# Kernel tuning notes

Measured on AMD Instinct MI355X. Metric: run time of the kernel, lower is better.

Reference implementation:

```python
import math
import jax, jax.numpy as jnp
import numpy as np

B, S, D, H, L, V = 4, 1024, 1024, 16, 12, 32000
DH = D // H
MAX_LEN = 5000


def _layernorm(x, g, b, eps=1e-5):
    mu = jnp.mean(x, axis=-1, keepdims=True)
    var = jnp.mean(jnp.square(x - mu), axis=-1, keepdims=True)
    return (x - mu) * jax.lax.rsqrt(var + eps) * g + b


def _make_pe():
    pos = np.arange(MAX_LEN, dtype=np.float32)[:, None]
    div = np.exp(np.arange(0, D, 2, dtype=np.float32) * (-math.log(10000.0) / D))
    pe = np.zeros((MAX_LEN, D), dtype=np.float32)
    pe[:, 0::2] = np.sin(pos * div)
    pe[:, 1::2] = np.cos(pos * div)
    return jnp.asarray(pe[:, None, :])  # [max_len, 1, D] as in the torch buffer


def setup_inputs() -> dict:
    key = jax.random.key(0)
    ks = jax.random.split(key, 8)
    X = jax.random.randint(ks[0], (B, S), 0, V)
    emb = jax.random.normal(ks[1], (V, D), dtype=jnp.float32) * 0.02
    pe = _make_pe()
    ln1_g = jnp.ones((L, D), jnp.float32)
    ln1_b = jnp.zeros((L, D), jnp.float32)
    wa = jax.random.normal(ks[2], (L, D, 3 * D), dtype=jnp.float32) * 0.02
    ba = jnp.zeros((L, 3 * D), jnp.float32)
    wp = jax.random.normal(ks[3], (L, D, D), dtype=jnp.float32) * 0.02
    bp = jnp.zeros((L, D), jnp.float32)
    ln2_g = jnp.ones((L, D), jnp.float32)
    ln2_b = jnp.zeros((L, D), jnp.float32)
    wf = jax.random.normal(ks[4], (L, D, D), dtype=jnp.float32) * 0.02
    bf = jnp.zeros((L, D), jnp.float32)
    wout = jax.random.normal(ks[5], (V, D), dtype=jnp.float32) * 0.02
    return dict(X=X, emb=emb, pe=pe, ln1_g=ln1_g, ln1_b=ln1_b, wa=wa, ba=ba,
                wp=wp, bp=bp, ln2_g=ln2_g, ln2_b=ln2_b, wf=wf, bf=bf, wout=wout)


def _block(x, ln1g, ln1b, wa_i, ba_i, wp_i, bp_i, ln2g, ln2b, wf_i, bf_i):
    h = _layernorm(x, ln1g, ln1b)               # post-ln1 value is the residual base
    qkv = h @ wa_i + ba_i                        # [B,S,3D]
    q, k, v = jnp.split(qkv, 3, axis=-1)
    def heads(t):
        return t.reshape(B, S, H, DH).transpose(0, 2, 1, 3)  # [B,H,S,DH]
    q, k, v = heads(q), heads(k), heads(v)
    scores = jnp.einsum('bhqd,bhkd->bhqk', q, k)  # NOTE: no 1/sqrt(d) scaling (scale=False)
    probs = jax.nn.softmax(scores, axis=-1)
    o = jnp.einsum('bhqk,bhkd->bhqd', probs, v)
    o = o.transpose(0, 2, 1, 3).reshape(B, S, D)
    attn_out = o @ wp_i + bp_i
    x = h + attn_out
    x = x + _layernorm(x, ln2g, ln2b) @ wf_i + bf_i
    return x


def reference(X, emb, pe, ln1_g, ln1_b, wa, ba, wp, bp, ln2_g, ln2_b, wf, bf, wout):
    x = emb[X] * math.sqrt(D)           # [B,S,D]
    x = x + pe[:B]                       # faithful: pe indexed by batch dim, broadcast over seq
    for i in range(L):
        x = _block(x, ln1_g[i], ln1_b[i], wa[i], ba[i], wp[i], bp[i],
                   ln2_g[i], ln2_b[i], wf[i], bf[i])
    logits = jnp.einsum('bsd,vd->bsv', x, wout)  # Linear(d, vocab, bias=False)
    return logits
```

## Files before the change

### kernel.cpp

```cpp
#include <hip/hip_runtime.h>
#include <hip/hip_bf16.h>

typedef __attribute__((ext_vector_type(4))) float f32x4;
typedef __attribute__((ext_vector_type(8))) short s16x8;
typedef __attribute__((ext_vector_type(4))) short s16x4;

constexpr int Bc = 4, Sc = 1024, Dc = 1024, Hc = 16, DHc = 64, Lc = 12, Vc = 32000;
constexpr int Tc = Bc * Sc;
constexpr int D3c = 3 * Dc;

static __device__ __forceinline__ short f2bf(float f) {
  union { float f; unsigned u; } v; v.f = f;
  unsigned r = (v.u + 0x7FFFu + ((v.u >> 16) & 1u)) >> 16;
  return (short)r;
}

__launch_bounds__(256)
__global__ void k_embed(const int* __restrict__ X, const float* __restrict__ emb,
                        const float* __restrict__ pe, float* __restrict__ x) {
  int row = blockIdx.x;
  int b = row >> 10;
  int tok = X[row];
  int t = threadIdx.x;
  float4 e = ((const float4*)(emb + (size_t)tok * Dc))[t];
  float4 p = ((const float4*)(pe + (size_t)b * Dc))[t];
  float4 r;
  r.x = e.x * 32.0f + p.x;  r.y = e.y * 32.0f + p.y;
  r.z = e.z * 32.0f + p.z;  r.w = e.w * 32.0f + p.w;
  ((float4*)(x + (size_t)row * Dc))[t] = r;
}

template<bool WF32>
__launch_bounds__(256)
__global__ void k_ln(const float* __restrict__ x, const float* __restrict__ g,
                     const float* __restrict__ be, float* __restrict__ hf,
                     short* __restrict__ hb) {
  int row = blockIdx.x, t = threadIdx.x;
  float4 v = ((const float4*)(x + (size_t)row * Dc))[t];
  float s1 = v.x + v.y + v.z + v.w;
  float s2 = v.x * v.x + v.y * v.y + v.z * v.z + v.w * v.w;
#pragma unroll
  for (int off = 1; off < 64; off <<= 1) {
    s1 += __shfl_xor(s1, off);
    s2 += __shfl_xor(s2, off);
  }
  __shared__ float a1[4], a2[4];
  if ((t & 63) == 0) { a1[t >> 6] = s1; a2[t >> 6] = s2; }
  __syncthreads();
  s1 = a1[0] + a1[1] + a1[2] + a1[3];
  s2 = a2[0] + a2[1] + a2[2] + a2[3];
  float mu = s1 * (1.0f / Dc);
  float var = s2 * (1.0f / Dc) - mu * mu;
  float rs = rsqrtf(var + 1e-5f);
  float4 gg = ((const float4*)g)[t];
  float4 bb = ((const float4*)be)[t];
  float4 r;
  r.x = (v.x - mu) * rs * gg.x + bb.x;
  r.y = (v.y - mu) * rs * gg.y + bb.y;
  r.z = (v.z - mu) * rs * gg.z + bb.z;
  r.w = (v.w - mu) * rs * gg.w + bb.w;
  if (WF32) ((float4*)(hf + (size_t)row * Dc))[t] = r;
  s16x4 o; o[0] = f2bf(r.x); o[1] = f2bf(r.y); o[2] = f2bf(r.z); o[3] = f2bf(r.w);
  ((s16x4*)(hb + (size_t)row * Dc))[t] = o;
}

__launch_bounds__(256)
__global__ void k_transpose_bf(const float* __restrict__ in0, short* __restrict__ out0,
                               int R, int C) {
  const float* in = in0 + (size_t)blockIdx.z * R * C;
  short* out = out0 + (size_t)blockIdx.z * R * C;
  __shared__ float tile[64][65];
  int c0 = blockIdx.x * 64, r0 = blockIdx.y * 64;
  int t = threadIdx.x;
#pragma unroll
  for (int e = 0; e < 16; ++e) {
    int idx = e * 256 + t;
    int r = idx >> 6, c = idx & 63;
    tile[r][c] = in[(size_t)(r0 + r) * C + c0 + c];
  }
  __syncthreads();
#pragma unroll
  for (int e = 0; e < 16; ++e) {
    int idx = e * 256 + t;
    int c = idx >> 6, r = idx & 63;
    out[(size_t)(c0 + c) * R + r0 + r] = f2bf(tile[r][c]);
  }
}

__launch_bounds__(256)
__global__ void k_f2bf(const float* __restrict__ in, short* __restrict__ out, size_t n) {
  size_t i = ((size_t)blockIdx.x * 256 + threadIdx.x) * 4;
  size_t stride = (size_t)gridDim.x * 1024;
  for (; i < n; i += stride) {
    float4 v = *(const float4*)(in + i);
    s16x4 r; r[0] = f2bf(v.x); r[1] = f2bf(v.y); r[2] = f2bf(v.z); r[3] = f2bf(v.w);
    *(s16x4*)(out + i) = r;
  }
}

template<int MODE, int SWZ>
__launch_bounds__(256)
__global__ void k_gemm(const short* __restrict__ A, const short* __restrict__ Bt,
                       const float* __restrict__ bias, const float* __restrict__ res,
                       void* __restrict__ Cout, int M, int N, int K, int nby) {
  __shared__ __align__(16) short Al[128][64];
  __shared__ __align__(16) short Bl[128][64];
  int bid = blockIdx.x;
  int by, bx;
  if (SWZ == 2) {
    int xcd = bid & 7, i = bid >> 3;
    by = xcd * 4 + (i & 3);
    bx = i >> 2;
  } else {
    by = bid % nby;
    bx = bid / nby;
  }
  int m0 = by * 128, n0 = bx * 128;
  int t = threadIdx.x;
  int w = t >> 6, lane = t & 63;
  int wr = w >> 1, wc = w & 1;
  int lg = lane >> 4, lr = lane & 15;

  int srow = t >> 3, sg = t & 7;
  int scol = ((sg ^ (srow & 7)) * 8);
  const short* ga = A + (size_t)(m0 + srow) * K + scol;
  const short* gb = Bt + (size_t)(n0 + srow) * K + scol;
  short* la = &Al[srow][sg * 8];
  short* lb = &Bl[srow][sg * 8];

  f32x4 acc[4][4];
#pragma unroll
  for (int i = 0; i < 4; ++i)
#pragma unroll
    for (int j = 0; j < 4; ++j) { acc[i][j][0] = 0.f; acc[i][j][1] = 0.f; acc[i][j][2] = 0.f; acc[i][j][3] = 0.f; }

  for (int k0 = 0; k0 < K; k0 += 64) {
#pragma unroll
    for (int i = 0; i < 4; ++i) {
      __builtin_amdgcn_global_load_lds(
          (const __attribute__((address_space(1))) void*)(ga + (size_t)(i * 32) * K + k0),
          (__attribute__((address_space(3))) void*)(la + i * 32 * 64), 16, 0, 0);
      __builtin_amdgcn_global_load_lds(
          (const __attribute__((address_space(1))) void*)(gb + (size_t)(i * 32) * K + k0),
          (__attribute__((address_space(3))) void*)(lb + i * 32 * 64), 16, 0, 0);
    }
    __syncthreads();
#pragma unroll
    for (int kk = 0; kk < 2; ++kk) {
      s16x8 af[4], bfr[4];
#pragma unroll
      for (int mi = 0; mi < 4; ++mi) {
        int row = wr * 64 + mi * 16 + lr;
        af[mi] = *(const s16x8*)&Al[row][((kk * 4 + lg) ^ (lr & 7)) * 8];
      }
#pragma unroll
      for (int ni = 0; ni < 4; ++ni) {
        int row = wc * 64 + ni * 16 + lr;
        bfr[ni] = *(const s16x8*)&Bl[row][((kk * 4 + lg) ^ (lr & 7)) * 8];
      }
#pragma unroll
      for (int mi = 0; mi < 4; ++mi)
#pragma unroll
        for (int ni = 0; ni < 4; ++ni)
          acc[mi][ni] = __builtin_amdgcn_mfma_f32_16x16x32_bf16(af[mi], bfr[ni], acc[mi][ni], 0, 0, 0);
    }
    __syncthreads();
  }
#pragma unroll
  for (int mi = 0; mi < 4; ++mi) {
#pragma unroll
    for (int ni = 0; ni < 4; ++ni) {
      int ncol = n0 + wc * 64 + ni * 16 + lr;
      float bv = (MODE == 2) ? 0.0f : bias[ncol];
      int mbase = m0 + wr * 64 + mi * 16 + lg * 4;
#pragma unroll
      for (int j = 0; j < 4; ++j) {
        size_t idx = (size_t)(mbase + j) * N + ncol;
        float vv = acc[mi][ni][j] + bv;
        if (MODE == 1) vv += res[idx];
        if (MODE == 0) ((short*)Cout)[idx] = f2bf(vv);
        else           ((float*)Cout)[idx] = vv;
      }
    }
  }
}

__launch_bounds__(256)
__global__ void k_attn(const short* __restrict__ qkv, short* __restrict__ obf) {
  int bh = blockIdx.x;
  int b = bh >> 4, h = bh & 15;
  int q0 = blockIdx.y * 64;
  int t = threadIdx.x, w = t >> 6, lane = t & 63;
  int lg = lane >> 4, lr = lane & 15;
  __shared__ __align__(16) short vls[64][72];
  __shared__ __align__(16) short pls[64][72];
  s16x8 qf0, qf1;
  {
    const short* qp = qkv + (size_t)(b * Sc + q0 + w * 16 + lr) * D3c + h * DHc + lg * 8;
    qf0 = *(const s16x8*)qp;
    qf1 = *(const s16x8*)(qp + 32);
  }
  float lsum[4] = {0.f, 0.f, 0.f, 0.f};
  f32x4 oacc[4];
#pragma unroll
  for (int f = 0; f < 4; ++f) { oacc[f][0] = 0.f; oacc[f][1] = 0.f; oacc[f][2] = 0.f; oacc[f][3] = 0.f; }

  int vsk = t >> 2, vdh = (t & 3) * 16;
  const short* vbase = qkv + (size_t)(b * Sc) * D3c + 2 * Dc + h * DHc;
  const short* kbase = qkv + (size_t)(b * Sc) * D3c + Dc + h * DHc;

  for (int kt = 0; kt < Sc / 64; ++kt) {
    int k0 = kt * 64;
    __syncthreads();
    {
      const short* vp = vbase + (size_t)(k0 + vsk) * D3c + vdh;
      s16x8 v0 = *(const s16x8*)vp;
      s16x8 v1 = *(const s16x8*)(vp + 8);
#pragma unroll
      for (int e = 0; e < 8; ++e) vls[vdh + e][vsk] = v0[e];
#pragma unroll
      for (int e = 0; e < 8; ++e) vls[vdh + 8 + e][vsk] = v1[e];
    }
    f32x4 sc[4];
#pragma unroll
    for (int f = 0; f < 4; ++f) {
      const short* kp = kbase + (size_t)(k0 + f * 16 + lr) * D3c + lg * 8;
      s16x8 kf0 = *(const s16x8*)kp;
      s16x8 kf1 = *(const s16x8*)(kp + 32);
      f32x4 c; c[0] = 0.f; c[1] = 0.f; c[2] = 0.f; c[3] = 0.f;
      c = __builtin_amdgcn_mfma_f32_16x16x32_bf16(qf0, kf0, c, 0, 0, 0);
      c = __builtin_amdgcn_mfma_f32_16x16x32_bf16(qf1, kf1, c, 0, 0, 0);
      sc[f] = c;
    }
#pragma unroll
    for (int f = 0; f < 4; ++f)
#pragma unroll
      for (int j = 0; j < 4; ++j) {
        float pv = __expf(sc[f][j]);
        lsum[j] += pv;
        pls[w * 16 + lg * 4 + j][f * 16 + lr] = f2bf(pv);
      }
    __syncthreads();
    s16x8 pa0 = *(const s16x8*)&pls[w * 16 + lr][lg * 8];
    s16x8 pa1 = *(const s16x8*)&pls[w * 16 + lr][32 + lg * 8];
#pragma unroll
    for (int f = 0; f < 4; ++f) {
      s16x8 vb0 = *(const s16x8*)&vls[f * 16 + lr][lg * 8];
      s16x8 vb1 = *(const s16x8*)&vls[f * 16 + lr][32 + lg * 8];
      oacc[f] = __builtin_amdgcn_mfma_f32_16x16x32_bf16(pa0, vb0, oacc[f], 0, 0, 0);
      oacc[f] = __builtin_amdgcn_mfma_f32_16x16x32_bf16(pa1, vb1, oacc[f], 0, 0, 0);
    }
  }
#pragma unroll
  for (int j = 0; j < 4; ++j) {
#pragma unroll
    for (int off = 1; off < 16; off <<= 1) lsum[j] += __shfl_xor(lsum[j], off);
  }
#pragma unroll
  for (int j = 0; j < 4; ++j) {
    float inv = 1.0f / lsum[j];
    int srow = q0 + w * 16 + lg * 4 + j;
#pragma unroll
    for (int f = 0; f < 4; ++f)
      obf[(size_t)(b * Sc + srow) * Dc + h * DHc + f * 16 + lr] = f2bf(oacc[f][j] * inv);
  }
}

extern "C" void kernel_launch(void* const* d_in, const int* in_sizes, int n_in,
                              void* d_out, int out_size, void* d_ws, size_t ws_size,
                              hipStream_t stream) {
  const int*   X    = (const int*)d_in[0];
  const float* emb  = (const float*)d_in[1];
  const float* pe   = (const float*)d_in[2];
  const float* ln1g = (const float*)d_in[3];
  const float* ln1b = (const float*)d_in[4];
  const float* wa   = (const float*)d_in[5];
  const float* ba   = (const float*)d_in[6];
  const float* wp   = (const float*)d_in[7];
  const float* bp   = (const float*)d_in[8];
  const float* ln2g = (const float*)d_in[9];
  const float* ln2b = (const float*)d_in[10];
  const float* wf   = (const float*)d_in[11];
  const float* bfv  = (const float*)d_in[12];
  const float* wout = (const float*)d_in[13];
  float* out = (float*)d_out;

  char* p = (char*)d_ws;
  float* x    = (float*)p; p += (size_t)Tc * Dc * 4;
  float* hx   = (float*)p; p += (size_t)Tc * Dc * 4;
  short* hbf  = (short*)p; p += (size_t)Tc * Dc * 2;
  short* l2bf = (short*)p; p += (size_t)Tc * Dc * 2;
  short* qkvb = (short*)p; p += (size_t)Tc * D3c * 2;
  short* obf  = (short*)p; p += (size_t)Tc * Dc * 2;
  short* xbf  = (short*)p; p += (size_t)Tc * Dc * 2;
  short* wat  = (short*)p; p += (size_t)Lc * D3c * Dc * 2;
  short* wpt  = (short*)p; p += (size_t)Lc * Dc * Dc * 2;
  short* wft  = (short*)p; p += (size_t)Lc * Dc * Dc * 2;
  short* woutb = (short*)p; p += (size_t)Vc * Dc * 2;

  k_transpose_bf<<<dim3(D3c / 64, Dc / 64, Lc), 256, 0, stream>>>(wa, wat, Dc, D3c);
  k_transpose_bf<<<dim3(Dc / 64, Dc / 64, Lc), 256, 0, stream>>>(wp, wpt, Dc, Dc);
  k_transpose_bf<<<dim3(Dc / 64, Dc / 64, Lc), 256, 0, stream>>>(wf, wft, Dc, Dc);
  k_f2bf<<<4096, 256, 0, stream>>>(wout, woutb, (size_t)Vc * Dc);

  k_embed<<<Tc, 256, 0, stream>>>(X, emb, pe, x);

  const int nby = Tc / 128;
  for (int l = 0; l < Lc; ++l) {
    k_ln<true><<<Tc, 256, 0, stream>>>(x, ln1g + l * Dc, ln1b + l * Dc, hx, hbf);
    k_gemm<0, 0><<<(D3c / 128) * nby, 256, 0, stream>>>(
        hbf, wat + (size_t)l * D3c * Dc, ba + l * D3c, nullptr, qkvb, Tc, D3c, Dc, nby);
    k_attn<<<dim3(Bc * Hc, Sc / 64), 256, 0, stream>>>(qkvb, obf);
    k_gemm<1, 0><<<(Dc / 128) * nby, 256, 0, stream>>>(
        obf, wpt + (size_t)l * Dc * Dc, bp + l * Dc, hx, x, Tc, Dc, Dc, nby);
    k_ln<false><<<Tc, 256, 0, stream>>>(x, ln2g + l * Dc, ln2b + l * Dc, nullptr, l2bf);
    k_gemm<1, 0><<<(Dc / 128) * nby, 256, 0, stream>>>(
        l2bf, wft + (size_t)l * Dc * Dc, bfv + l * Dc, x, x, Tc, Dc, Dc, nby);
  }

  k_f2bf<<<2048, 256, 0, stream>>>(x, xbf, (size_t)Tc * Dc);
  k_gemm<2, 2><<<(Vc / 128) * nby, 256, 0, stream>>>(
      xbf, woutb, nullptr, nullptr, out, Tc, Vc, Dc, nby);
}
```

Baseline: 3.480 ms.

## Transpose attention MFMA operands for vectorized LDS stores and output writes

The attention kernel swaps the MFMA operand order to compute S^T and O^T. Each lane now owns a single query row, so P can be stored to LDS as 4-wide packed vectors, the row sum needs only two cross-lane shuffles, and output is written as 8-byte vectors. The V transpose into LDS now uses four 8-byte row loads repacked into 4-wide stores instead of scalar 2-byte scattered stores. This is meant to cut LDS store instructions and bank conflicts in the attention inner loop, at the cost of narrower global loads for V.

```diff
diff --git a/kernel.cpp b/kernel.cpp
--- a/kernel.cpp
+++ b/kernel.cpp
@@ -200,69 +200,64 @@
     qf0 = *(const s16x8*)qp;
     qf1 = *(const s16x8*)(qp + 32);
   }
-  float lsum[4] = {0.f, 0.f, 0.f, 0.f};
+  float lsum = 0.0f;
   f32x4 oacc[4];
 #pragma unroll
   for (int f = 0; f < 4; ++f) { oacc[f][0] = 0.f; oacc[f][1] = 0.f; oacc[f][2] = 0.f; oacc[f][3] = 0.f; }
 
-  int vsk = t >> 2, vdh = (t & 3) * 16;
-  const short* vbase = qkv + (size_t)(b * Sc) * D3c + 2 * Dc + h * DHc;
+  int va = t & 15;
+  int vb = t >> 4;
+  const short* vbase = qkv + (size_t)(b * Sc) * D3c + 2 * Dc + h * DHc + vb * 4;
   const short* kbase = qkv + (size_t)(b * Sc) * D3c + Dc + h * DHc;
 
   for (int kt = 0; kt < Sc / 64; ++kt) {
     int k0 = kt * 64;
     __syncthreads();
     {
-      const short* vp = vbase + (size_t)(k0 + vsk) * D3c + vdh;
-      s16x8 v0 = *(const s16x8*)vp;
-      s16x8 v1 = *(const s16x8*)(vp + 8);
-#pragma unroll
-      for (int e = 0; e < 8; ++e) vls[vdh + e][vsk] = v0[e];
-#pragma unroll
-      for (int e = 0; e < 8; ++e) vls[vdh + 8 + e][vsk] = v1[e];
-    }
-    f32x4 sc[4];
+      s16x4 ld0 = *(const s16x4*)(vbase + (size_t)(k0 + va * 4 + 0) * D3c);
+      s16x4 ld1 = *(const s16x4*)(vbase + (size_t)(k0 + va * 4 + 1) * D3c);
+      s16x4 ld2 = *(const s16x4*)(vbase + (size_t)(k0 + va * 4 + 2) * D3c);
+      s16x4 ld3 = *(const s16x4*)(vbase + (size_t)(k0 + va * 4 + 3) * D3c);
+#pragma unroll
+      for (int e = 0; e < 4; ++e) {
+        s16x4 pk; pk[0] = ld0[e]; pk[1] = ld1[e]; pk[2] = ld2[e]; pk[3] = ld3[e];
+        *(s16x4*)&vls[vb * 4 + e][va * 4] = pk;
+      }
+    }
 #pragma unroll
     for (int f = 0; f < 4; ++f) {
       const short* kp = kbase + (size_t)(k0 + f * 16 + lr) * D3c + lg * 8;
       s16x8 kf0 = *(const s16x8*)kp;
       s16x8 kf1 = *(const s16x8*)(kp + 32);
       f32x4 c; c[0] = 0.f; c[1] = 0.f; c[2] = 0.f; c[3] = 0.f;
-      c = __builtin_amdgcn_mfma_f32_16x16x32_bf16(qf0, kf0, c, 0, 0, 0);
-      c = __builtin_amdgcn_mfma_f32_16x16x32_bf16(qf1, kf1, c, 0, 0, 0);
-      sc[f] = c;
-    }
-#pragma unroll
-    for (int f = 0; f < 4; ++f)
-#pragma unroll
-      for (int j = 0; j < 4; ++j) {
-        float pv = __expf(sc[f][j]);
-        lsum[j] += pv;
-        pls[w * 16 + lg * 4 + j][f * 16 + lr] = f2bf(pv);
-      }
+      c = __builtin_amdgcn_mfma_f32_16x16x32_bf16(kf0, qf0, c, 0, 0, 0);
+      c = __builtin_amdgcn_mfma_f32_16x16x32_bf16(kf1, qf1, c, 0, 0, 0);
+      float p0 = __expf(c[0]), p1 = __expf(c[1]), p2 = __expf(c[2]), p3 = __expf(c[3]);
+      lsum += (p0 + p1) + (p2 + p3);
+      s16x4 pk; pk[0] = f2bf(p0); pk[1] = f2bf(p1); pk[2] = f2bf(p2); pk[3] = f2bf(p3);
+      *(s16x4*)&pls[w * 16 + lr][f * 16 + lg * 4] = pk;
+    }
     __syncthreads();
-    s16x8 pa0 = *(const s16x8*)&pls[w * 16 + lr][lg * 8];
-    s16x8 pa1 = *(const s16x8*)&pls[w * 16 + lr][32 + lg * 8];
+    s16x8 pb0 = *(const s16x8*)&pls[w * 16 + lr][lg * 8];
+    s16x8 pb1 = *(const s16x8*)&pls[w * 16 + lr][32 + lg * 8];
 #pragma unroll
     for (int f = 0; f < 4; ++f) {
-      s16x8 vb0 = *(const s16x8*)&vls[f * 16 + lr][lg * 8];
-      s16x8 vb1 = *(const s16x8*)&vls[f * 16 + lr][32 + lg * 8];
-      oacc[f] = __builtin_amdgcn_mfma_f32_16x16x32_bf16(pa0, vb0, oacc[f], 0, 0, 0);
-      oacc[f] = __builtin_amdgcn_mfma_f32_16x16x32_bf16(pa1, vb1, oacc[f], 0, 0, 0);
-    }
-  }
-#pragma unroll
-  for (int j = 0; j < 4; ++j) {
-#pragma unroll
-    for (int off = 1; off < 16; off <<= 1) lsum[j] += __shfl_xor(lsum[j], off);
-  }
-#pragma unroll
-  for (int j = 0; j < 4; ++j) {
-    float inv = 1.0f / lsum[j];
-    int srow = q0 + w * 16 + lg * 4 + j;
-#pragma unroll
-    for (int f = 0; f < 4; ++f)
-      obf[(size_t)(b * Sc + srow) * Dc + h * DHc + f * 16 + lr] = f2bf(oacc[f][j] * inv);
+      s16x8 af0 = *(const s16x8*)&vls[f * 16 + lr][lg * 8];
+      s16x8 af1 = *(const s16x8*)&vls[f * 16 + lr][32 + lg * 8];
+      oacc[f] = __builtin_amdgcn_mfma_f32_16x16x32_bf16(af0, pb0, oacc[f], 0, 0, 0);
+      oacc[f] = __builtin_amdgcn_mfma_f32_16x16x32_bf16(af1, pb1, oacc[f], 0, 0, 0);
+    }
+  }
+  lsum += __shfl_xor(lsum, 16);
+  lsum += __shfl_xor(lsum, 32);
+  float inv = 1.0f / lsum;
+  int qrow = q0 + w * 16 + lr;
+#pragma unroll
+  for (int f = 0; f < 4; ++f) {
+    s16x4 ok;
+#pragma unroll
+    for (int j = 0; j < 4; ++j) ok[j] = f2bf(oacc[f][j] * inv);
+    *(s16x4*)(obf + (size_t)(b * Sc + qrow) * Dc + h * DHc + f * 16 + lg * 4) = ok;
   }
 }
 
```

Result: slower. 3.749 ms (+7.7%).
